# Kernel tuning notes

Measured on AMD Instinct MI355X. Metric: run time of the kernel, lower is better.

The kernel has to match this reference:

```python
import jax, jax.numpy as jnp
import numpy as np

B, D, P, K_ROUTE = 131072, 256, 16, 4


def setup_inputs() -> dict:
    key = jax.random.key(0)
    ks = jax.random.split(key, 12)
    w_scale = 0.02
    return {
        "z_n": jax.random.normal(ks[0], (B, D), dtype=jnp.float32),
        "z_sea": jax.random.normal(ks[1], (B, D), dtype=jnp.float32),
        "z_trend": jax.random.normal(ks[2], (B, D), dtype=jnp.float32),
        "noise_z": jax.random.normal(ks[3], (B, D), dtype=jnp.float32),   # randn_like(z_fused)
        "noise_r": jax.random.normal(ks[4], (B, P), dtype=jnp.float32),   # randn_like(routing_logits)
        "patch_candidates": jax.random.randint(ks[5], (P,), 1, 64, dtype=jnp.int32),
        "W_proj": jax.random.normal(ks[6], (D, 3 * D), dtype=jnp.float32) * w_scale,
        "b_proj": jnp.zeros((D,), dtype=jnp.float32),
        "W_route": jax.random.normal(ks[7], (P, D), dtype=jnp.float32) * w_scale,
        "b_route": jnp.zeros((P,), dtype=jnp.float32),
        "W_noise": jax.random.normal(ks[8], (P, D), dtype=jnp.float32) * w_scale,
        "b_noise": jnp.zeros((P,), dtype=jnp.float32),
    }


def reference(z_n, z_sea, z_trend, noise_z, noise_r, patch_candidates,
              W_proj, b_proj, W_route, b_route, W_noise, b_noise):
    # feature fusion: Linear(3D -> D) on concat
    z_concat = jnp.concatenate([z_n, z_sea, z_trend], axis=-1)        # [B, 3D]
    z_fused = z_concat @ W_proj.T + b_proj                            # [B, D]
    gating_input = z_fused + noise_z * 0.1                            # noise injection 1
    routing_logits = gating_input @ W_route.T + b_route               # [B, P]
    noise_scale = jax.nn.softplus(gating_input @ W_noise.T + b_noise)  # [B, P]
    routing_logits = routing_logits + noise_r * noise_scale           # noise injection 2
    routing_weights = jax.nn.softmax(routing_logits, axis=-1)         # [B, P]
    top_k_values, top_k_indices = jax.lax.top_k(routing_weights, K_ROUTE)  # [B, K]
    rows = jnp.arange(routing_weights.shape[0])[:, None]
    sparse_routing = jnp.zeros_like(routing_weights).at[rows, top_k_indices].set(top_k_values)
    selected_patches = patch_candidates[top_k_indices]                # [B, K]
    return (sparse_routing, selected_patches, top_k_indices)
```

## Files before the change

### kernel.cpp

```cpp
#include <hip/hip_runtime.h>
#include <math.h>

#define B_ROWS 131072
#define ROWS 128
#define XPB 40
#define LP 34

typedef __attribute__((ext_vector_type(8))) short short8v;
typedef __attribute__((ext_vector_type(4))) short short4v;
typedef __attribute__((ext_vector_type(4))) float float4v;

__device__ __forceinline__ short f2bf(float x) {
  unsigned u = __builtin_bit_cast(unsigned, x);
  u += 0x7fffu + ((u >> 16) & 1u);
  return (short)(u >> 16);
}
__device__ __forceinline__ float bf2f(short h) {
  unsigned u = ((unsigned)(unsigned short)h) << 16;
  return __builtin_bit_cast(float, u);
}

__global__ void precompute_M(const float* __restrict__ Wp,
                             const float* __restrict__ Wr,
                             const float* __restrict__ Wn,
                             const float* __restrict__ bp,
                             const float* __restrict__ br,
                             const float* __restrict__ bn,
                             float* __restrict__ M,
                             float* __restrict__ c) {
  int o = blockIdx.x * 256 + threadIdx.x;
  if (o < 32 * 1024) {
    int j = o >> 10, k = o & 1023;
    const float* W = (j < 16) ? Wr : Wn;
    int jj = j & 15;
    float v;
    if (k < 768) {
      double s0 = 0.0, s1 = 0.0, s2 = 0.0, s3 = 0.0;
      for (int d = 0; d < 256; d += 4) {
        s0 += (double)W[jj * 256 + d]     * (double)Wp[(d)     * 768 + k];
        s1 += (double)W[jj * 256 + d + 1] * (double)Wp[(d + 1) * 768 + k];
        s2 += (double)W[jj * 256 + d + 2] * (double)Wp[(d + 2) * 768 + k];
        s3 += (double)W[jj * 256 + d + 3] * (double)Wp[(d + 3) * 768 + k];
      }
      v = (float)((s0 + s1) + (s2 + s3));
    } else {
      v = 0.1f * W[jj * 256 + (k - 768)];
    }
    M[o] = v;
  }
  if (blockIdx.x == 0 && threadIdx.x < 32) {
    int j = threadIdx.x, jj = j & 15;
    const float* W = (j < 16) ? Wr : Wn;
    const float* b = (j < 16) ? br : bn;
    double s = (double)b[jj];
    for (int d = 0; d < 256; ++d)
      s += (double)W[jj * 256 + d] * (double)bp[d];
    c[j] = (float)s;
  }
}

#define LOAD_STAGE(S_) do {                                                   \
    const int k0_ = (S_) * 32;                                                \
    const float* src_; int col0_;                                             \
    if (k0_ < 256)      { src_ = zn; col0_ = k0_; }                           \
    else if (k0_ < 512) { src_ = zs; col0_ = k0_ - 256; }                     \
    else if (k0_ < 768) { src_ = zt; col0_ = k0_ - 512; }                     \
    else                { src_ = nz; col0_ = k0_ - 768; }                     \
    const float* base_ = src_ + (size_t)(row0 + sr) * 256 + col0_ + 4 * sk4;  \
    xg0 = *(const float4*)(base_);                                            \
    xg1 = *(const float4*)(base_ + 32 * 256);                                 \
    xg2 = *(const float4*)(base_ + 64 * 256);                                 \
    xg3 = *(const float4*)(base_ + 96 * 256);                                 \
    mg  = *(const float4*)&M[(size_t)sr * 1024 + k0_ + 4 * sk4];              \
  } while (0)

#define CVT3(VG_, PH_, PM_, PL_, OFF_) do {                                   \
    short4v h_, m_, l_;                                                       \
    float v_, r_;                                                             \
    v_ = VG_.x; h_[0] = f2bf(v_); r_ = v_ - bf2f(h_[0]);                      \
    m_[0] = f2bf(r_); l_[0] = f2bf(r_ - bf2f(m_[0]));                         \
    v_ = VG_.y; h_[1] = f2bf(v_); r_ = v_ - bf2f(h_[1]);                      \
    m_[1] = f2bf(r_); l_[1] = f2bf(r_ - bf2f(m_[1]));                         \
    v_ = VG_.z; h_[2] = f2bf(v_); r_ = v_ - bf2f(h_[2]);                      \
    m_[2] = f2bf(r_); l_[2] = f2bf(r_ - bf2f(m_[2]));                         \
    v_ = VG_.w; h_[3] = f2bf(v_); r_ = v_ - bf2f(h_[3]);                      \
    m_[3] = f2bf(r_); l_[3] = f2bf(r_ - bf2f(m_[3]));                         \
    *(short4v*)&PH_[OFF_] = h_;                                               \
    *(short4v*)&PM_[OFF_] = m_;                                               \
    *(short4v*)&PL_[OFF_] = l_;                                               \
  } while (0)

__global__ __launch_bounds__(256, 3)
void router_main(const float* __restrict__ zn, const float* __restrict__ zs,
                 const float* __restrict__ zt, const float* __restrict__ nz,
                 const float* __restrict__ nr, const int* __restrict__ patches,
                 const float* __restrict__ M, const float* __restrict__ c,
                 float* __restrict__ out) {
  __shared__ __align__(16) char smem[38400];
  short* const Xh  = (short*)smem;
  short* const Xm  = (short*)(smem + 10240);
  short* const Xl  = (short*)(smem + 20480);
  short* const Mhs = (short*)(smem + 30720);
  short* const Mms = (short*)(smem + 33280);
  short* const Mls = (short*)(smem + 35840);
  float* const Ls  = (float*)smem;

  const int t = threadIdx.x;
  const int row0 = blockIdx.x * ROWS;
  const int sr = t >> 3;
  const int sk4 = t & 7;
  const int lane = t & 63;
  const int w = t >> 6;

  float4v aB00 = {0,0,0,0}, aB01 = {0,0,0,0}, aB10 = {0,0,0,0}, aB11 = {0,0,0,0};
  float4v aS00 = {0,0,0,0}, aS01 = {0,0,0,0}, aS10 = {0,0,0,0}, aS11 = {0,0,0,0};
  double d00[4], d01[4], d10[4], d11[4];
#pragma unroll
  for (int r = 0; r < 4; ++r) { d00[r] = 0.0; d01[r] = 0.0; d10[r] = 0.0; d11[r] = 0.0; }

  float4 xg0, xg1, xg2, xg3, mg;

  const int aoff = (w * 32 + (lane & 15)) * XPB + (lane >> 4) * 8;
  const int boff = (lane & 15) * XPB + (lane >> 4) * 8;
  const int soff = sr * XPB + 4 * sk4;

  LOAD_STAGE(0);

  for (int s = 0; s < 32; ++s) {
    __syncthreads();
    CVT3(xg0, Xh, Xm, Xl, soff);
    CVT3(xg1, Xh, Xm, Xl, soff + 32 * XPB);
    CVT3(xg2, Xh, Xm, Xl, soff + 64 * XPB);
    CVT3(xg3, Xh, Xm, Xl, soff + 96 * XPB);
    CVT3(mg, Mhs, Mms, Mls, soff);
    __syncthreads();

    if (s < 31) LOAD_STAGE(s + 1);

    short8v ah0 = *(const short8v*)&Xh[aoff];
    short8v ah1 = *(const short8v*)&Xh[aoff + 16 * XPB];
    short8v am0 = *(const short8v*)&Xm[aoff];
    short8v am1 = *(const short8v*)&Xm[aoff + 16 * XPB];
    short8v al0 = *(const short8v*)&Xl[aoff];
    short8v al1 = *(const short8v*)&Xl[aoff + 16 * XPB];
    short8v bh0 = *(const short8v*)&Mhs[boff];
    short8v bh1 = *(const short8v*)&Mhs[boff + 16 * XPB];
    short8v bm0 = *(const short8v*)&Mms[boff];
    short8v bm1 = *(const short8v*)&Mms[boff + 16 * XPB];
    short8v bl0 = *(const short8v*)&Mls[boff];
    short8v bl1 = *(const short8v*)&Mls[boff + 16 * XPB];

    aB00 = __builtin_amdgcn_mfma_f32_16x16x32_bf16(ah0, bh0, aB00, 0, 0, 0);
    aB01 = __builtin_amdgcn_mfma_f32_16x16x32_bf16(ah0, bh1, aB01, 0, 0, 0);
    aB10 = __builtin_amdgcn_mfma_f32_16x16x32_bf16(ah1, bh0, aB10, 0, 0, 0);
    aB11 = __builtin_amdgcn_mfma_f32_16x16x32_bf16(ah1, bh1, aB11, 0, 0, 0);
    aS00 = __builtin_amdgcn_mfma_f32_16x16x32_bf16(ah0, bm0, aS00, 0, 0, 0);
    aS01 = __builtin_amdgcn_mfma_f32_16x16x32_bf16(ah0, bm1, aS01, 0, 0, 0);
    aS10 = __builtin_amdgcn_mfma_f32_16x16x32_bf16(ah1, bm0, aS10, 0, 0, 0);
    aS11 = __builtin_amdgcn_mfma_f32_16x16x32_bf16(ah1, bm1, aS11, 0, 0, 0);
    aS00 = __builtin_amdgcn_mfma_f32_16x16x32_bf16(am0, bh0, aS00, 0, 0, 0);
    aS01 = __builtin_amdgcn_mfma_f32_16x16x32_bf16(am0, bh1, aS01, 0, 0, 0);
    aS10 = __builtin_amdgcn_mfma_f32_16x16x32_bf16(am1, bh0, aS10, 0, 0, 0);
    aS11 = __builtin_amdgcn_mfma_f32_16x16x32_bf16(am1, bh1, aS11, 0, 0, 0);
    aS00 = __builtin_amdgcn_mfma_f32_16x16x32_bf16(ah0, bl0, aS00, 0, 0, 0);
    aS01 = __builtin_amdgcn_mfma_f32_16x16x32_bf16(ah0, bl1, aS01, 0, 0, 0);
    aS10 = __builtin_amdgcn_mfma_f32_16x16x32_bf16(ah1, bl0, aS10, 0, 0, 0);
    aS11 = __builtin_amdgcn_mfma_f32_16x16x32_bf16(ah1, bl1, aS11, 0, 0, 0);
    aS00 = __builtin_amdgcn_mfma_f32_16x16x32_bf16(al0, bh0, aS00, 0, 0, 0);
    aS01 = __builtin_amdgcn_mfma_f32_16x16x32_bf16(al0, bh1, aS01, 0, 0, 0);
    aS10 = __builtin_amdgcn_mfma_f32_16x16x32_bf16(al1, bh0, aS10, 0, 0, 0);
    aS11 = __builtin_amdgcn_mfma_f32_16x16x32_bf16(al1, bh1, aS11, 0, 0, 0);
    aS00 = __builtin_amdgcn_mfma_f32_16x16x32_bf16(am0, bm0, aS00, 0, 0, 0);
    aS01 = __builtin_amdgcn_mfma_f32_16x16x32_bf16(am0, bm1, aS01, 0, 0, 0);
    aS10 = __builtin_amdgcn_mfma_f32_16x16x32_bf16(am1, bm0, aS10, 0, 0, 0);
    aS11 = __builtin_amdgcn_mfma_f32_16x16x32_bf16(am1, bm1, aS11, 0, 0, 0);

#pragma unroll
    for (int r = 0; r < 4; ++r) {
      d00[r] += (double)aB00[r] + (double)aS00[r]; aB00[r] = 0.f; aS00[r] = 0.f;
      d01[r] += (double)aB01[r] + (double)aS01[r]; aB01[r] = 0.f; aS01[r] = 0.f;
      d10[r] += (double)aB10[r] + (double)aS10[r]; aB10[r] = 0.f; aS10[r] = 0.f;
      d11[r] += (double)aB11[r] + (double)aS11[r]; aB11[r] = 0.f; aS11[r] = 0.f;
    }
  }

  __syncthreads();

  {
    const double c0 = (double)c[lane & 15];
    const double c1 = (double)c[16 + (lane & 15)];
    const int er = w * 32 + (lane >> 4) * 4;
    const int jc = lane & 15;
#pragma unroll
    for (int reg = 0; reg < 4; ++reg) {
      Ls[(er + reg) * LP + jc]           = (float)(d00[reg] + c0);
      Ls[(er + reg) * LP + 16 + jc]      = (float)(d01[reg] + c1);
      Ls[(er + 16 + reg) * LP + jc]      = (float)(d10[reg] + c0);
      Ls[(er + 16 + reg) * LP + 16 + jc] = (float)(d11[reg] + c1);
    }
  }
  __syncthreads();

  if (t < ROWS) {
    const int row = row0 + t;
    float L[32];
#pragma unroll
    for (int j = 0; j < 32; ++j) L[j] = Ls[t * LP + j];

    float nrv[16];
#pragma unroll
    for (int q = 0; q < 4; ++q) {
      float4 v = *(const float4*)&nr[(size_t)row * 16 + 4 * q];
      nrv[4 * q] = v.x; nrv[4 * q + 1] = v.y; nrv[4 * q + 2] = v.z; nrv[4 * q + 3] = v.w;
    }

    float lg[16];
#pragma unroll
    for (int p = 0; p < 16; ++p) {
      const float x = L[16 + p];
      const float sp = (x > 15.f) ? x : log1pf(expf(x));
      lg[p] = L[p] + nrv[p] * sp;
    }

    float mx = lg[0];
#pragma unroll
    for (int p = 1; p < 16; ++p) mx = fmaxf(mx, lg[p]);
    float e[16]; float sum = 0.f;
#pragma unroll
    for (int p = 0; p < 16; ++p) { e[p] = expf(lg[p] - mx); sum += e[p]; }
    float w2[16];
#pragma unroll
    for (int p = 0; p < 16; ++p) w2[p] = e[p] / sum;

    int idx[4]; float val[4]; unsigned used = 0;
#pragma unroll
    for (int kk = 0; kk < 4; ++kk) {
      float best = -1.f; int bi = 0;
#pragma unroll
      for (int p = 0; p < 16; ++p) {
        const bool ok = (((used >> p) & 1u) == 0u) && (w2[p] > best);
        best = ok ? w2[p] : best;
        bi = ok ? p : bi;
      }
      idx[kk] = bi; val[kk] = best; used |= (1u << bi);
    }

    float so[16];
#pragma unroll
    for (int p = 0; p < 16; ++p) {
      float v = 0.f;
#pragma unroll
      for (int kk = 0; kk < 4; ++kk) v = (idx[kk] == p) ? val[kk] : v;
      so[p] = v;
    }
#pragma unroll
    for (int q = 0; q < 4; ++q)
      *(float4*)&out[(size_t)row * 16 + 4 * q] =
          make_float4(so[4 * q], so[4 * q + 1], so[4 * q + 2], so[4 * q + 3]);

    float4 pv, iv;
    pv.x = (float)patches[idx[0]]; pv.y = (float)patches[idx[1]];
    pv.z = (float)patches[idx[2]]; pv.w = (float)patches[idx[3]];
    iv.x = (float)idx[0]; iv.y = (float)idx[1];
    iv.z = (float)idx[2]; iv.w = (float)idx[3];
    *(float4*)&out[(size_t)B_ROWS * 16 + (size_t)row * 4] = pv;
    *(float4*)&out[(size_t)B_ROWS * 20 + (size_t)row * 4] = iv;
  }
}

extern "C" void kernel_launch(void* const* d_in, const int* in_sizes, int n_in,
                              void* d_out, int out_size, void* d_ws, size_t ws_size,
                              hipStream_t stream) {
  const float* zn = (const float*)d_in[0];
  const float* zs = (const float*)d_in[1];
  const float* zt = (const float*)d_in[2];
  const float* nz = (const float*)d_in[3];
  const float* nr = (const float*)d_in[4];
  const int*   pc = (const int*)d_in[5];
  const float* Wp = (const float*)d_in[6];
  const float* bp = (const float*)d_in[7];
  const float* Wr = (const float*)d_in[8];
  const float* br = (const float*)d_in[9];
  const float* Wn = (const float*)d_in[10];
  const float* bn = (const float*)d_in[11];
  float* out = (float*)d_out;
  float* M = (float*)d_ws;
  float* c = M + 32 * 1024;

  precompute_M<<<128, 256, 0, stream>>>(Wp, Wr, Wn, bp, br, bn, M, c);
  router_main<<<B_ROWS / ROWS, 256, 0, stream>>>(zn, zs, zt, nz, nr, pc, M, c, out);
}
```

Before: 501.3 us.

## Double-buffer global loads, truncate bf16 splits, keep small terms in fp32

Splits each fp32 value into bf16 hi/mid/lo pieces by masking bits instead of round-to-nearest conversion. This cuts the ALU work in the conversion step. Global loads are now double-buffered in registers two stages ahead, giving more memory latency hiding at the cost of extra registers under a 3-blocks-per-SM launch bound. The small correction-term accumulators are no longer flushed to double each stage but summed across the whole K loop in fp32. That removes per-stage double-precision adds but slightly reduces accuracy, which could change top-k picks near ties.

```diff
diff --git a/kernel.cpp b/kernel.cpp
--- a/kernel.cpp
+++ b/kernel.cpp
@@ -7,18 +7,7 @@
 #define LP 34
 
 typedef __attribute__((ext_vector_type(8))) short short8v;
-typedef __attribute__((ext_vector_type(4))) short short4v;
 typedef __attribute__((ext_vector_type(4))) float float4v;
-
-__device__ __forceinline__ short f2bf(float x) {
-  unsigned u = __builtin_bit_cast(unsigned, x);
-  u += 0x7fffu + ((u >> 16) & 1u);
-  return (short)(u >> 16);
-}
-__device__ __forceinline__ float bf2f(short h) {
-  unsigned u = ((unsigned)(unsigned short)h) << 16;
-  return __builtin_bit_cast(float, u);
-}
 
 __global__ void precompute_M(const float* __restrict__ Wp,
                              const float* __restrict__ Wr,
@@ -59,7 +48,8 @@
   }
 }
 
-#define LOAD_STAGE(S_) do {                                                   \
+
+#define LOAD_INTO(S_, X0_, X1_, X2_, X3_, MG_) do {                           \
     const int k0_ = (S_) * 32;                                                \
     const float* src_; int col0_;                                             \
     if (k0_ < 256)      { src_ = zn; col0_ = k0_; }                           \
@@ -67,27 +57,88 @@
     else if (k0_ < 768) { src_ = zt; col0_ = k0_ - 512; }                     \
     else                { src_ = nz; col0_ = k0_ - 768; }                     \
     const float* base_ = src_ + (size_t)(row0 + sr) * 256 + col0_ + 4 * sk4;  \
-    xg0 = *(const float4*)(base_);                                            \
-    xg1 = *(const float4*)(base_ + 32 * 256);                                 \
-    xg2 = *(const float4*)(base_ + 64 * 256);                                 \
-    xg3 = *(const float4*)(base_ + 96 * 256);                                 \
-    mg  = *(const float4*)&M[(size_t)sr * 1024 + k0_ + 4 * sk4];              \
+    X0_ = *(const float4*)(base_);                                            \
+    X1_ = *(const float4*)(base_ + 32 * 256);                                 \
+    X2_ = *(const float4*)(base_ + 64 * 256);                                 \
+    X3_ = *(const float4*)(base_ + 96 * 256);                                 \
+    MG_ = *(const float4*)&M[(size_t)sr * 1024 + k0_ + 4 * sk4];              \
+  } while (0)
+
+#define SPLIT1(V_, H_, M_, L_) do {                                           \
+    unsigned u_ = __builtin_bit_cast(unsigned, V_);                           \
+    H_ = u_ & 0xFFFF0000u;                                                    \
+    float r_ = (V_) - __builtin_bit_cast(float, H_);                          \
+    unsigned ru_ = __builtin_bit_cast(unsigned, r_);                          \
+    M_ = ru_ & 0xFFFF0000u;                                                   \
+    float r2_ = r_ - __builtin_bit_cast(float, M_);                          \
+    L_ = __builtin_bit_cast(unsigned, r2_);   \
   } while (0)
 
 #define CVT3(VG_, PH_, PM_, PL_, OFF_) do {                                   \
-    short4v h_, m_, l_;                                                       \
-    float v_, r_;                                                             \
-    v_ = VG_.x; h_[0] = f2bf(v_); r_ = v_ - bf2f(h_[0]);                      \
-    m_[0] = f2bf(r_); l_[0] = f2bf(r_ - bf2f(m_[0]));                         \
-    v_ = VG_.y; h_[1] = f2bf(v_); r_ = v_ - bf2f(h_[1]);                      \
-    m_[1] = f2bf(r_); l_[1] = f2bf(r_ - bf2f(m_[1]));                         \
-    v_ = VG_.z; h_[2] = f2bf(v_); r_ = v_ - bf2f(h_[2]);                      \
-    m_[2] = f2bf(r_); l_[2] = f2bf(r_ - bf2f(m_[2]));                         \
-    v_ = VG_.w; h_[3] = f2bf(v_); r_ = v_ - bf2f(h_[3]);                      \
-    m_[3] = f2bf(r_); l_[3] = f2bf(r_ - bf2f(m_[3]));                         \
-    *(short4v*)&PH_[OFF_] = h_;                                               \
-    *(short4v*)&PM_[OFF_] = m_;                                               \
-    *(short4v*)&PL_[OFF_] = l_;                                               \
+    unsigned h0_,h1_,h2_,h3_,m0_,m1_,m2_,m3_,l0_,l1_,l2_,l3_;                 \
+    SPLIT1(VG_.x, h0_, m0_, l0_); SPLIT1(VG_.y, h1_, m1_, l1_);               \
+    SPLIT1(VG_.z, h2_, m2_, l2_); SPLIT1(VG_.w, h3_, m3_, l3_);               \
+    uint2 ph_, pm_, pl_;                                                      \
+    ph_.x = (h0_ >> 16) | h1_;  ph_.y = (h2_ >> 16) | h3_;                    \
+    pm_.x = (m0_ >> 16) | m1_;  pm_.y = (m2_ >> 16) | m3_;                    \
+    pl_.x = (l0_ >> 16) | l1_;  pl_.y = (l2_ >> 16) | l3_;                    \
+    *(uint2*)&PH_[OFF_] = ph_;                                                \
+    *(uint2*)&PM_[OFF_] = pm_;                                                \
+    *(uint2*)&PL_[OFF_] = pl_;                                                \
+  } while (0)
+
+#define WRITE_STAGE(X0_, X1_, X2_, X3_, MG_) do {                             \
+    CVT3(X0_, Xh, Xm, Xl, soff);                                              \
+    CVT3(X1_, Xh, Xm, Xl, soff + 32 * XPB);                                   \
+    CVT3(X2_, Xh, Xm, Xl, soff + 64 * XPB);                                   \
+    CVT3(X3_, Xh, Xm, Xl, soff + 96 * XPB);                                   \
+    CVT3(MG_, Mhs, Mms, Mls, soff);                                           \
+  } while (0)
+
+#define COMPUTE_STAGE() do {                                                  \
+    short8v ah0 = *(const short8v*)&Xh[aoff];                                 \
+    short8v ah1 = *(const short8v*)&Xh[aoff + 16 * XPB];                      \
+    short8v am0 = *(const short8v*)&Xm[aoff];                                 \
+    short8v am1 = *(const short8v*)&Xm[aoff + 16 * XPB];                      \
+    short8v al0 = *(const short8v*)&Xl[aoff];                                 \
+    short8v al1 = *(const short8v*)&Xl[aoff + 16 * XPB];                      \
+    short8v bh0 = *(const short8v*)&Mhs[boff];                                \
+    short8v bh1 = *(const short8v*)&Mhs[boff + 16 * XPB];                     \
+    short8v bm0 = *(const short8v*)&Mms[boff];                                \
+    short8v bm1 = *(const short8v*)&Mms[boff + 16 * XPB];                     \
+    short8v bl0 = *(const short8v*)&Mls[boff];                                \
+    short8v bl1 = *(const short8v*)&Mls[boff + 16 * XPB];                     \
+    aB00 = __builtin_amdgcn_mfma_f32_16x16x32_bf16(ah0, bh0, aB00, 0, 0, 0);  \
+    aB01 = __builtin_amdgcn_mfma_f32_16x16x32_bf16(ah0, bh1, aB01, 0, 0, 0);  \
+    aB10 = __builtin_amdgcn_mfma_f32_16x16x32_bf16(ah1, bh0, aB10, 0, 0, 0);  \
+    aB11 = __builtin_amdgcn_mfma_f32_16x16x32_bf16(ah1, bh1, aB11, 0, 0, 0);  \
+    aS00 = __builtin_amdgcn_mfma_f32_16x16x32_bf16(ah0, bm0, aS00, 0, 0, 0);  \
+    aS01 = __builtin_amdgcn_mfma_f32_16x16x32_bf16(ah0, bm1, aS01, 0, 0, 0);  \
+    aS10 = __builtin_amdgcn_mfma_f32_16x16x32_bf16(ah1, bm0, aS10, 0, 0, 0);  \
+    aS11 = __builtin_amdgcn_mfma_f32_16x16x32_bf16(ah1, bm1, aS11, 0, 0, 0);  \
+    aS00 = __builtin_amdgcn_mfma_f32_16x16x32_bf16(am0, bh0, aS00, 0, 0, 0);  \
+    aS01 = __builtin_amdgcn_mfma_f32_16x16x32_bf16(am0, bh1, aS01, 0, 0, 0);  \
+    aS10 = __builtin_amdgcn_mfma_f32_16x16x32_bf16(am1, bh0, aS10, 0, 0, 0);  \
+    aS11 = __builtin_amdgcn_mfma_f32_16x16x32_bf16(am1, bh1, aS11, 0, 0, 0);  \
+    aS00 = __builtin_amdgcn_mfma_f32_16x16x32_bf16(ah0, bl0, aS00, 0, 0, 0);  \
+    aS01 = __builtin_amdgcn_mfma_f32_16x16x32_bf16(ah0, bl1, aS01, 0, 0, 0);  \
+    aS10 = __builtin_amdgcn_mfma_f32_16x16x32_bf16(ah1, bl0, aS10, 0, 0, 0);  \
+    aS11 = __builtin_amdgcn_mfma_f32_16x16x32_bf16(ah1, bl1, aS11, 0, 0, 0);  \
+    aS00 = __builtin_amdgcn_mfma_f32_16x16x32_bf16(al0, bh0, aS00, 0, 0, 0);  \
+    aS01 = __builtin_amdgcn_mfma_f32_16x16x32_bf16(al0, bh1, aS01, 0, 0, 0);  \
+    aS10 = __builtin_amdgcn_mfma_f32_16x16x32_bf16(al1, bh0, aS10, 0, 0, 0);  \
+    aS11 = __builtin_amdgcn_mfma_f32_16x16x32_bf16(al1, bh1, aS11, 0, 0, 0);  \
+    aS00 = __builtin_amdgcn_mfma_f32_16x16x32_bf16(am0, bm0, aS00, 0, 0, 0);  \
+    aS01 = __builtin_amdgcn_mfma_f32_16x16x32_bf16(am0, bm1, aS01, 0, 0, 0);  \
+    aS10 = __builtin_amdgcn_mfma_f32_16x16x32_bf16(am1, bm0, aS10, 0, 0, 0);  \
+    aS11 = __builtin_amdgcn_mfma_f32_16x16x32_bf16(am1, bm1, aS11, 0, 0, 0);  \
+    _Pragma("unroll")                                                         \
+    for (int r = 0; r < 4; ++r) {       \
+      d00[r] += (double)aB00[r]; aB00[r] = 0.f;                               \
+      d01[r] += (double)aB01[r]; aB01[r] = 0.f;                               \
+      d10[r] += (double)aB10[r]; aB10[r] = 0.f;                               \
+      d11[r] += (double)aB11[r]; aB11[r] = 0.f;                               \
+    }                                                                         \
   } while (0)
 
 __global__ __launch_bounds__(256, 3)
@@ -118,70 +169,28 @@
 #pragma unroll
   for (int r = 0; r < 4; ++r) { d00[r] = 0.0; d01[r] = 0.0; d10[r] = 0.0; d11[r] = 0.0; }
 
-  float4 xg0, xg1, xg2, xg3, mg;
+  float4 xa0, xa1, xa2, xa3, ma;
+  float4 xb0, xb1, xb2, xb3, mb;
 
   const int aoff = (w * 32 + (lane & 15)) * XPB + (lane >> 4) * 8;
   const int boff = (lane & 15) * XPB + (lane >> 4) * 8;
   const int soff = sr * XPB + 4 * sk4;
 
-  LOAD_STAGE(0);
-
-  for (int s = 0; s < 32; ++s) {
+  LOAD_INTO(0, xa0, xa1, xa2, xa3, ma);
+  LOAD_INTO(1, xb0, xb1, xb2, xb3, mb);
+
+  for (int s = 0; s < 32; s += 2) {
     __syncthreads();
-    CVT3(xg0, Xh, Xm, Xl, soff);
-    CVT3(xg1, Xh, Xm, Xl, soff + 32 * XPB);
-    CVT3(xg2, Xh, Xm, Xl, soff + 64 * XPB);
-    CVT3(xg3, Xh, Xm, Xl, soff + 96 * XPB);
-    CVT3(mg, Mhs, Mms, Mls, soff);
+    WRITE_STAGE(xa0, xa1, xa2, xa3, ma);
     __syncthreads();
-
-    if (s < 31) LOAD_STAGE(s + 1);
-
-    short8v ah0 = *(const short8v*)&Xh[aoff];
-    short8v ah1 = *(const short8v*)&Xh[aoff + 16 * XPB];
-    short8v am0 = *(const short8v*)&Xm[aoff];
-    short8v am1 = *(const short8v*)&Xm[aoff + 16 * XPB];
-    short8v al0 = *(const short8v*)&Xl[aoff];
-    short8v al1 = *(const short8v*)&Xl[aoff + 16 * XPB];
-    short8v bh0 = *(const short8v*)&Mhs[boff];
-    short8v bh1 = *(const short8v*)&Mhs[boff + 16 * XPB];
-    short8v bm0 = *(const short8v*)&Mms[boff];
-    short8v bm1 = *(const short8v*)&Mms[boff + 16 * XPB];
-    short8v bl0 = *(const short8v*)&Mls[boff];
-    short8v bl1 = *(const short8v*)&Mls[boff + 16 * XPB];
-
-    aB00 = __builtin_amdgcn_mfma_f32_16x16x32_bf16(ah0, bh0, aB00, 0, 0, 0);
-    aB01 = __builtin_amdgcn_mfma_f32_16x16x32_bf16(ah0, bh1, aB01, 0, 0, 0);
-    aB10 = __builtin_amdgcn_mfma_f32_16x16x32_bf16(ah1, bh0, aB10, 0, 0, 0);
-    aB11 = __builtin_amdgcn_mfma_f32_16x16x32_bf16(ah1, bh1, aB11, 0, 0, 0);
-    aS00 = __builtin_amdgcn_mfma_f32_16x16x32_bf16(ah0, bm0, aS00, 0, 0, 0);
-    aS01 = __builtin_amdgcn_mfma_f32_16x16x32_bf16(ah0, bm1, aS01, 0, 0, 0);
-    aS10 = __builtin_amdgcn_mfma_f32_16x16x32_bf16(ah1, bm0, aS10, 0, 0, 0);
-    aS11 = __builtin_amdgcn_mfma_f32_16x16x32_bf16(ah1, bm1, aS11, 0, 0, 0);
-    aS00 = __builtin_amdgcn_mfma_f32_16x16x32_bf16(am0, bh0, aS00, 0, 0, 0);
-    aS01 = __builtin_amdgcn_mfma_f32_16x16x32_bf16(am0, bh1, aS01, 0, 0, 0);
-    aS10 = __builtin_amdgcn_mfma_f32_16x16x32_bf16(am1, bh0, aS10, 0, 0, 0);
-    aS11 = __builtin_amdgcn_mfma_f32_16x16x32_bf16(am1, bh1, aS11, 0, 0, 0);
-    aS00 = __builtin_amdgcn_mfma_f32_16x16x32_bf16(ah0, bl0, aS00, 0, 0, 0);
-    aS01 = __builtin_amdgcn_mfma_f32_16x16x32_bf16(ah0, bl1, aS01, 0, 0, 0);
-    aS10 = __builtin_amdgcn_mfma_f32_16x16x32_bf16(ah1, bl0, aS10, 0, 0, 0);
-    aS11 = __builtin_amdgcn_mfma_f32_16x16x32_bf16(ah1, bl1, aS11, 0, 0, 0);
-    aS00 = __builtin_amdgcn_mfma_f32_16x16x32_bf16(al0, bh0, aS00, 0, 0, 0);
-    aS01 = __builtin_amdgcn_mfma_f32_16x16x32_bf16(al0, bh1, aS01, 0, 0, 0);
-    aS10 = __builtin_amdgcn_mfma_f32_16x16x32_bf16(al1, bh0, aS10, 0, 0, 0);
-    aS11 = __builtin_amdgcn_mfma_f32_16x16x32_bf16(al1, bh1, aS11, 0, 0, 0);
-    aS00 = __builtin_amdgcn_mfma_f32_16x16x32_bf16(am0, bm0, aS00, 0, 0, 0);
-    aS01 = __builtin_amdgcn_mfma_f32_16x16x32_bf16(am0, bm1, aS01, 0, 0, 0);
-    aS10 = __builtin_amdgcn_mfma_f32_16x16x32_bf16(am1, bm0, aS10, 0, 0, 0);
-    aS11 = __builtin_amdgcn_mfma_f32_16x16x32_bf16(am1, bm1, aS11, 0, 0, 0);
-
-#pragma unroll
-    for (int r = 0; r < 4; ++r) {
-      d00[r] += (double)aB00[r] + (double)aS00[r]; aB00[r] = 0.f; aS00[r] = 0.f;
-      d01[r] += (double)aB01[r] + (double)aS01[r]; aB01[r] = 0.f; aS01[r] = 0.f;
-      d10[r] += (double)aB10[r] + (double)aS10[r]; aB10[r] = 0.f; aS10[r] = 0.f;
-      d11[r] += (double)aB11[r] + (double)aS11[r]; aB11[r] = 0.f; aS11[r] = 0.f;
-    }
+    if (s + 2 < 32) LOAD_INTO(s + 2, xa0, xa1, xa2, xa3, ma);
+    COMPUTE_STAGE();
+
+    __syncthreads();
+    WRITE_STAGE(xb0, xb1, xb2, xb3, mb);
+    __syncthreads();
+    if (s + 3 < 32) LOAD_INTO(s + 3, xb0, xb1, xb2, xb3, mb);
+    COMPUTE_STAGE();
   }
 
   __syncthreads();
@@ -193,10 +202,10 @@
     const int jc = lane & 15;
 #pragma unroll
     for (int reg = 0; reg < 4; ++reg) {
-      Ls[(er + reg) * LP + jc]           = (float)(d00[reg] + c0);
-      Ls[(er + reg) * LP + 16 + jc]      = (float)(d01[reg] + c1);
-      Ls[(er + 16 + reg) * LP + jc]      = (float)(d10[reg] + c0);
-      Ls[(er + 16 + reg) * LP + 16 + jc] = (float)(d11[reg] + c1);
+      Ls[(er + reg) * LP + jc]           = (float)(d00[reg] + (double)aS00[reg] + c0);
+      Ls[(er + reg) * LP + 16 + jc]      = (float)(d01[reg] + (double)aS01[reg] + c1);
+      Ls[(er + 16 + reg) * LP + jc]      = (float)(d10[reg] + (double)aS10[reg] + c0);
+      Ls[(er + 16 + reg) * LP + 16 + jc] = (float)(d11[reg] + (double)aS11[reg] + c1);
     }
   }
   __syncthreads();
```

Result: slower. 528.0 us (+5.3%).
